# Kernel optimization log

Hardware: AMD Instinct MI355X
Metric: run time of the kernel (lower is better)

Reference implementation:

```python
import jax, jax.numpy as jnp
import numpy as np

TEMPERATURE = 0.07
EPS = 1e-12  # F.normalize clamp


def _project(x, We, be, W1, b1, W2, b2):
    # encoder Linear then projection head Linear->ReLU->Linear
    h = x @ We + be                      # [B, 512]
    h = jax.nn.relu(h @ W1 + b1)         # [B, 256]
    return h @ W2 + b2                   # [B, 128]


def _ntxent(z1, z2, t):
    B = z1.shape[0]
    z1 = z1 / jnp.maximum(jnp.linalg.norm(z1, axis=1, keepdims=True), EPS)
    z2 = z2 / jnp.maximum(jnp.linalg.norm(z2, axis=1, keepdims=True), EPS)
    reps = jnp.concatenate([z1, z2], axis=0)          # [2B, 128]
    sim = reps @ reps.T                               # [2B, 2B]
    N = 2 * B
    idx = jnp.arange(N)
    # positives: eye rolled by B along columns -> column (i+B) mod N
    pos = sim[idx, (idx + B) % N][:, None]            # [N, 1]
    # negatives: all off-diagonal entries per row, in column order
    cols = jnp.arange(N - 1)[None, :]                 # [1, N-1]
    neg_idx = cols + (cols >= idx[:, None])           # skip the diagonal
    neg = jnp.take_along_axis(sim, neg_idx, axis=1)   # [N, N-1]
    logits = jnp.concatenate([pos, neg], axis=1) / t  # [N, N]
    # cross-entropy with label 0
    return jnp.mean(jax.nn.logsumexp(logits, axis=1) - logits[:, 0])


def setup_inputs() -> dict:
    key = jax.random.key(0)
    ks = jax.random.split(key, 10)
    B, Din, Denc, Dh, Dp = 4096, 1024, 512, 256, 128
    s = lambda fan_in: 1.0 / np.sqrt(fan_in)
    return {
        "x_image": jax.random.normal(ks[0], (B, Din), jnp.float32),
        "x_text": jax.random.normal(ks[1], (B, Din), jnp.float32),
        "We_img": jax.random.normal(ks[2], (Din, Denc), jnp.float32) * s(Din),
        "be_img": jnp.zeros((Denc,), jnp.float32),
        "We_txt": jax.random.normal(ks[3], (Din, Denc), jnp.float32) * s(Din),
        "be_txt": jnp.zeros((Denc,), jnp.float32),
        "Wp1_img": jax.random.normal(ks[4], (Denc, Dh), jnp.float32) * s(Denc),
        "bp1_img": jnp.zeros((Dh,), jnp.float32),
        "Wp2_img": jax.random.normal(ks[5], (Dh, Dp), jnp.float32) * s(Dh),
        "bp2_img": jnp.zeros((Dp,), jnp.float32),
        "Wp1_txt": jax.random.normal(ks[6], (Denc, Dh), jnp.float32) * s(Denc),
        "bp1_txt": jnp.zeros((Dh,), jnp.float32),
        "Wp2_txt": jax.random.normal(ks[7], (Dh, Dp), jnp.float32) * s(Dh),
        "bp2_txt": jnp.zeros((Dp,), jnp.float32),
    }


def reference(x_image, x_text, We_img, be_img, We_txt, be_txt,
              Wp1_img, bp1_img, Wp2_img, bp2_img,
              Wp1_txt, bp1_txt, Wp2_txt, bp2_txt):
    z1 = _project(x_image, We_img, be_img, Wp1_img, bp1_img, Wp2_img, bp2_img)
    z2 = _project(x_text, We_txt, be_txt, Wp1_txt, bp1_txt, Wp2_txt, bp2_txt)
    # single modality pair ('image','text') -> one NT-Xent loss
    return _ntxent(z1, z2, TEMPERATURE)
```

## Files before the change

### kernel.cpp

```cpp
#include <hip/hip_runtime.h>
#include <hip/hip_bf16.h>
#include <math.h>

typedef __bf16 bf16_t;
typedef __bf16 bf8 __attribute__((ext_vector_type(8)));
typedef __bf16 bf4 __attribute__((ext_vector_type(4)));
typedef __bf16 bf16x2 __attribute__((ext_vector_type(2)));
typedef float f32x4 __attribute__((ext_vector_type(4)));

#define AS1 __attribute__((address_space(1)))
#define AS3 __attribute__((address_space(3)))

#define B_ROWS 4096
#define NTOT   8192
#define DIN    1024
#define DENC   512
#define DH     256
#define DP     128
#define INV_T        14.285714285714286f
#define SCALE_LOG2   20.609929155556620f

__device__ __forceinline__ f32x4 mfma_16x16x32(bf8 a, bf8 b, f32x4 c) {
  return __builtin_amdgcn_mfma_f32_16x16x32_bf16(a, b, c, 0, 0, 0);
}

__global__ __launch_bounds__(256) void prep_kernel(
    const float* __restrict__ x_i, const float* __restrict__ x_t,
    const float* __restrict__ We_i, const float* __restrict__ We_t,
    const float* __restrict__ W1_i, const float* __restrict__ W1_t,
    const float* __restrict__ W2_i, const float* __restrict__ W2_t,
    bf16_t* __restrict__ xb_i, bf16_t* __restrict__ xb_t,
    bf16_t* __restrict__ Wet_i, bf16_t* __restrict__ Wet_t,
    bf16_t* __restrict__ W1t_i, bf16_t* __restrict__ W1t_t,
    bf16_t* __restrict__ W2t_i, bf16_t* __restrict__ W2t_t) {
  const int b = blockIdx.x;
  const int tid = threadIdx.x;
  if (b >= 336) {
    int idx = (b - 336) * 256 + tid;
    const int HALF = (B_ROWS * DIN) / 4;
    const float* s; bf16_t* d; int off;
    if (idx < HALF) { s = x_i; d = xb_i; off = idx; }
    else            { s = x_t; d = xb_t; off = idx - HALF; }
    float4 v = ((const float4*)s)[off];
    bf4 w = { (bf16_t)v.x, (bf16_t)v.y, (bf16_t)v.z, (bf16_t)v.w };
    ((bf4*)d)[off] = w;
    return;
  }
  const float* src; bf16_t* dst; int K, N, tile;
  if (b < 128)      { src = We_i; dst = Wet_i; K = 1024; N = 512; tile = b; }
  else if (b < 256) { src = We_t; dst = Wet_t; K = 1024; N = 512; tile = b - 128; }
  else if (b < 288) { src = W1_i; dst = W1t_i; K = 512;  N = 256; tile = b - 256; }
  else if (b < 320) { src = W1_t; dst = W1t_t; K = 512;  N = 256; tile = b - 288; }
  else if (b < 328) { src = W2_i; dst = W2t_i; K = 256;  N = 128; tile = b - 320; }
  else              { src = W2_t; dst = W2t_t; K = 256;  N = 128; tile = b - 328; }
  const int tilesN = N >> 6;
  const int k0 = (tile / tilesN) * 64;
  const int n0 = (tile % tilesN) * 64;

  __shared__ float ld[64][65];
  #pragma unroll
  for (int i = 0; i < 4; ++i) {
    int cid = tid + i * 256;
    int r = cid >> 4;
    int c = (cid & 15) * 4;
    float4 v = *(const float4*)(src + (size_t)(k0 + r) * N + n0 + c);
    ld[r][c + 0] = v.x; ld[r][c + 1] = v.y; ld[r][c + 2] = v.z; ld[r][c + 3] = v.w;
  }
  __syncthreads();
  #pragma unroll
  for (int i = 0; i < 2; ++i) {
    int cid = tid + i * 256;
    int rn = cid >> 3;
    int c8 = (cid & 7) * 8;
    bf8 w;
    #pragma unroll
    for (int j = 0; j < 8; ++j) w[j] = (bf16_t)ld[c8 + j][rn];
    *(bf8*)(dst + (size_t)(n0 + rn) * K + k0 + c8) = w;
  }
}

template<int MT, bool RELU>
__global__ __launch_bounds__(256) void gemm_glds(
    const bf16_t* __restrict__ A0, const bf16_t* __restrict__ A1,
    const bf16_t* __restrict__ B0, const bf16_t* __restrict__ B1,
    const float* __restrict__ bias0, const float* __restrict__ bias1,
    bf16_t* __restrict__ out0, bf16_t* __restrict__ out1,
    int N, int K) {
  const bf16_t* A   = blockIdx.z ? A1 : A0;
  const bf16_t* Bt  = blockIdx.z ? B1 : B0;
  const float* bias = blockIdx.z ? bias1 : bias0;
  bf16_t* outp      = blockIdx.z ? out1 : out0;

  const int nb   = blockIdx.x * 64;
  const int mb   = blockIdx.y * MT;
  const int tid  = threadIdx.x;
  const int wave = tid >> 6;
  const int lane = tid & 63;
  const int l15  = lane & 15;
  const int quad = lane >> 4;
  constexpr int CH = MT / 64;

  __shared__ __align__(16) bf16_t As[MT * 32];
  __shared__ __align__(16) bf16_t Bs[64 * 32];

  f32x4 acc[CH][4];
  #pragma unroll
  for (int i = 0; i < CH; ++i)
    #pragma unroll
    for (int j = 0; j < 4; ++j) acc[i][j] = (f32x4){0.f, 0.f, 0.f, 0.f};

  for (int k0 = 0; k0 < K; k0 += 32) {
    __syncthreads();
    #pragma unroll
    for (int i = 0; i < CH; ++i) {
      const int s = tid + i * 256;
      const bf16_t* ga = A + (size_t)(mb + (s >> 2)) * K + k0 + (s & 3) * 8;
      __builtin_amdgcn_global_load_lds(
          (const AS1 void*)ga,
          (AS3 void*)(As + (size_t)(wave * 64 + i * 256) * 8), 16, 0, 0);
    }
    {
      const int s = tid;
      const bf16_t* gb = Bt + (size_t)(nb + (s >> 2)) * K + k0 + (s & 3) * 8;
      __builtin_amdgcn_global_load_lds(
          (const AS1 void*)gb,
          (AS3 void*)(Bs + (size_t)(wave * 64) * 8), 16, 0, 0);
    }
    __syncthreads();

    bf8 a[CH];
    #pragma unroll
    for (int i = 0; i < CH; ++i)
      a[i] = *(const bf8*)(As + (size_t)(wave * (16 * CH) + i * 16 + l15) * 32 + quad * 8);
    #pragma unroll
    for (int nt = 0; nt < 4; ++nt) {
      bf8 bb = *(const bf8*)(Bs + (size_t)(nt * 16 + l15) * 32 + quad * 8);
      #pragma unroll
      for (int i = 0; i < CH; ++i)
        acc[i][nt] = mfma_16x16x32(a[i], bb, acc[i][nt]);
    }
  }

  #pragma unroll
  for (int i = 0; i < CH; ++i) {
    const int orow = mb + wave * (16 * CH) + i * 16 + quad * 4;
    #pragma unroll
    for (int nt = 0; nt < 4; ++nt) {
      const int ocol = nb + nt * 16 + l15;
      const float bval = bias[ocol];
      #pragma unroll
      for (int r = 0; r < 4; ++r) {
        float v = acc[i][nt][r] + bval;
        if (RELU) v = fmaxf(v, 0.f);
        outp[(size_t)(orow + r) * N + ocol] = (bf16_t)v;
      }
    }
  }
}

__global__ __launch_bounds__(256) void head2_norm(
    const bf16_t* __restrict__ A0, const bf16_t* __restrict__ A1,
    const bf16_t* __restrict__ B0, const bf16_t* __restrict__ B1,
    const float* __restrict__ bias0, const float* __restrict__ bias1,
    bf16_t* __restrict__ reps) {
  const bf16_t* A   = blockIdx.z ? A1 : A0;
  const bf16_t* Bt  = blockIdx.z ? B1 : B0;
  const float* bias = blockIdx.z ? bias1 : bias0;

  const int mb   = blockIdx.x * 64;
  const int tid  = threadIdx.x;
  const int wave = tid >> 6;
  const int lane = tid & 63;
  const int l15  = lane & 15;
  const int quad = lane >> 4;

  __shared__ __align__(16) bf16_t As[64][40];
  __shared__ __align__(16) bf16_t Bs[128][40];

  f32x4 acc[8];
  #pragma unroll
  for (int i = 0; i < 8; ++i) acc[i] = (f32x4){0.f, 0.f, 0.f, 0.f};

  const int arow   = tid >> 2;
  const int achunk = (tid & 3) << 3;
  const bf16_t* Ap = A + (size_t)(mb + arow) * DH + achunk;

  for (int k0 = 0; k0 < DH; k0 += 32) {
    uint4 av = *(const uint4*)(Ap + k0);
    uint4 bv[2];
    #pragma unroll
    for (int i = 0; i < 2; ++i) {
      int cid = tid + i * 256;
      int br = cid >> 2, bc = (cid & 3) << 3;
      bv[i] = *(const uint4*)(Bt + (size_t)br * DH + k0 + bc);
    }
    __syncthreads();
    *(uint4*)&As[arow][achunk] = av;
    #pragma unroll
    for (int i = 0; i < 2; ++i) {
      int cid = tid + i * 256;
      int br = cid >> 2, bc = (cid & 3) << 3;
      *(uint4*)&Bs[br][bc] = bv[i];
    }
    __syncthreads();
    bf8 af = *(const bf8*)&As[wave * 16 + l15][quad * 8];
    #pragma unroll
    for (int nt = 0; nt < 8; ++nt) {
      bf8 bfv = *(const bf8*)&Bs[nt * 16 + l15][quad * 8];
      acc[nt] = mfma_16x16x32(af, bfv, acc[nt]);
    }
  }

  #pragma unroll
  for (int nt = 0; nt < 8; ++nt) {
    const float bval = bias[nt * 16 + l15];
    #pragma unroll
    for (int r = 0; r < 4; ++r) acc[nt][r] += bval;
  }
  const size_t rowbase = (size_t)(blockIdx.z ? B_ROWS : 0) + mb + wave * 16 + quad * 4;
  #pragma unroll
  for (int r = 0; r < 4; ++r) {
    float ss = 0.f;
    #pragma unroll
    for (int nt = 0; nt < 8; ++nt) ss += acc[nt][r] * acc[nt][r];
    ss += __shfl_xor(ss, 1);
    ss += __shfl_xor(ss, 2);
    ss += __shfl_xor(ss, 4);
    ss += __shfl_xor(ss, 8);
    const float inv = 1.0f / fmaxf(sqrtf(ss), 1e-12f);
    #pragma unroll
    for (int nt = 0; nt < 8; ++nt)
      reps[(rowbase + r) * DP + nt * 16 + l15] = (bf16_t)(acc[nt][r] * inv);
  }
}

__global__ __launch_bounds__(256) void sim_rowsum_kernel(
    const bf16_t* __restrict__ reps, float* __restrict__ S) {
  const int rowbase = blockIdx.y * 128;
  const int col0    = blockIdx.x * 512;
  const int tid  = threadIdx.x;
  const int wave = tid >> 6;
  const int lane = tid & 63;
  const int l15  = lane & 15;
  const int quad = lane >> 4;

  __shared__ __align__(16) bf16_t Bs[2][64 * DP];

  const int r0 = rowbase + wave * 32;
  bf8 af0[4], af1[4];
  #pragma unroll
  for (int kt = 0; kt < 4; ++kt) {
    af0[kt] = *(const bf8*)(reps + (size_t)(r0 + l15)      * DP + kt * 32 + quad * 8);
    af1[kt] = *(const bf8*)(reps + (size_t)(r0 + 16 + l15) * DP + kt * 32 + quad * 8);
  }

  float rs0[4] = {0.f, 0.f, 0.f, 0.f};
  float rs1[4] = {0.f, 0.f, 0.f, 0.f};

  for (int t = 0; t < 8; ++t) {
    bf16_t* buf = Bs[t & 1];
    __syncthreads();
    const int jt0 = col0 + t * 64;
    #pragma unroll
    for (int r = 0; r < 4; ++r) {
      const int s   = r * 256 + tid;
      const int col = s >> 4;
      const int cf  = (s & 15) ^ (col & 15);
      const bf16_t* g = reps + (size_t)(jt0 + col) * DP + cf * 8;
      __builtin_amdgcn_global_load_lds(
          (const AS1 void*)g,
          (AS3 void*)(buf + (size_t)(r * 256 + wave * 64) * 8), 16, 0, 0);
    }
    __syncthreads();

    #pragma unroll
    for (int st = 0; st < 4; ++st) {
      const bf16_t* base = buf + (size_t)(st * 16 + l15) * DP;
      bf8 b0 = *(const bf8*)(base + (((0 * 4 + quad) ^ l15) * 8));
      bf8 b1 = *(const bf8*)(base + (((1 * 4 + quad) ^ l15) * 8));
      bf8 b2 = *(const bf8*)(base + (((2 * 4 + quad) ^ l15) * 8));
      bf8 b3 = *(const bf8*)(base + (((3 * 4 + quad) ^ l15) * 8));
      f32x4 acc0 = (f32x4){0.f, 0.f, 0.f, 0.f};
      f32x4 acc1 = (f32x4){0.f, 0.f, 0.f, 0.f};
      acc0 = mfma_16x16x32(af0[0], b0, acc0); acc1 = mfma_16x16x32(af1[0], b0, acc1);
      acc0 = mfma_16x16x32(af0[1], b1, acc0); acc1 = mfma_16x16x32(af1[1], b1, acc1);
      acc0 = mfma_16x16x32(af0[2], b2, acc0); acc1 = mfma_16x16x32(af1[2], b2, acc1);
      acc0 = mfma_16x16x32(af0[3], b3, acc0); acc1 = mfma_16x16x32(af1[3], b3, acc1);
      #pragma unroll
      for (int r = 0; r < 4; ++r) {
        rs0[r] += __builtin_amdgcn_exp2f(acc0[r] * SCALE_LOG2);
        rs1[r] += __builtin_amdgcn_exp2f(acc1[r] * SCALE_LOG2);
      }
    }
  }

  const int i0 = r0 + quad * 4;
  #pragma unroll
  for (int r = 0; r < 4; ++r) {
    float v = rs0[r];
    v += __shfl_xor(v, 1); v += __shfl_xor(v, 2);
    v += __shfl_xor(v, 4); v += __shfl_xor(v, 8);
    if (l15 == 0) atomicAdd(&S[i0 + r], v);
  }
  #pragma unroll
  for (int r = 0; r < 4; ++r) {
    float v = rs1[r];
    v += __shfl_xor(v, 1); v += __shfl_xor(v, 2);
    v += __shfl_xor(v, 4); v += __shfl_xor(v, 8);
    if (l15 == 0) atomicAdd(&S[i0 + 16 + r], v);
  }
}

__global__ __launch_bounds__(256) void rowfinal_kernel(
    const bf16_t* __restrict__ reps, const float* __restrict__ S,
    float* __restrict__ Lsum, int* __restrict__ cnt,
    float* __restrict__ out) {
  const int tid  = threadIdx.x;
  const int wave = tid >> 6;
  const int lane = tid & 63;
  float part = 0.f;
  #pragma unroll 1
  for (int i = 0; i < 16; ++i) {
    const int row = blockIdx.x * 64 + wave * 16 + i;
    bf16x2 a = *(const bf16x2*)(reps + (size_t)row * DP + lane * 2);
    bf16x2 b = *(const bf16x2*)(reps + (size_t)(row ^ B_ROWS) * DP + lane * 2);
    float a0 = (float)a.x, a1 = (float)a.y;
    float b0 = (float)b.x, b1 = (float)b.y;
    float dii = a0 * a0 + a1 * a1;
    float pos = a0 * b0 + a1 * b1;
    #pragma unroll
    for (int m = 1; m < 64; m <<= 1) {
      dii += __shfl_xor(dii, m);
      pos += __shfl_xor(pos, m);
    }
    if (lane == 0) {
      float Si = S[row] - __builtin_amdgcn_exp2f(dii * SCALE_LOG2)
                        + __builtin_amdgcn_exp2f(pos * SCALE_LOG2);
      part += logf(Si) - pos * INV_T;
    }
  }
  __shared__ float wpart[4];
  if (lane == 0) wpart[wave] = part;
  __syncthreads();
  if (tid == 0) {
    float bsum = wpart[0] + wpart[1] + wpart[2] + wpart[3];
    atomicAdd(Lsum, bsum);
    __threadfence();
    int old = __hip_atomic_fetch_add(cnt, 1, __ATOMIC_ACQ_REL,
                                     __HIP_MEMORY_SCOPE_AGENT);
    if (old == (int)gridDim.x - 1) {
      float tot = __hip_atomic_load(Lsum, __ATOMIC_RELAXED,
                                    __HIP_MEMORY_SCOPE_AGENT);
      out[0] = tot * (1.0f / NTOT);
    }
  }
}

extern "C" void kernel_launch(void* const* d_in, const int* in_sizes, int n_in,
                              void* d_out, int out_size, void* d_ws, size_t ws_size,
                              hipStream_t stream) {
  const float* x_img  = (const float*)d_in[0];
  const float* x_txt  = (const float*)d_in[1];
  const float* We_img = (const float*)d_in[2];
  const float* be_img = (const float*)d_in[3];
  const float* We_txt = (const float*)d_in[4];
  const float* be_txt = (const float*)d_in[5];
  const float* W1_img = (const float*)d_in[6];
  const float* b1_img = (const float*)d_in[7];
  const float* W2_img = (const float*)d_in[8];
  const float* b2_img = (const float*)d_in[9];
  const float* W1_txt = (const float*)d_in[10];
  const float* b1_txt = (const float*)d_in[11];
  const float* W2_txt = (const float*)d_in[12];
  const float* b2_txt = (const float*)d_in[13];

  char* p = (char*)d_ws;
  bf16_t* xbf_img = (bf16_t*)p; p += (size_t)B_ROWS * DIN * 2;
  bf16_t* xbf_txt = (bf16_t*)p; p += (size_t)B_ROWS * DIN * 2;
  bf16_t* Wet_img = (bf16_t*)p; p += (size_t)DENC * DIN * 2;
  bf16_t* Wet_txt = (bf16_t*)p; p += (size_t)DENC * DIN * 2;
  bf16_t* W1t_img = (bf16_t*)p; p += (size_t)DH * DENC * 2;
  bf16_t* W1t_txt = (bf16_t*)p; p += (size_t)DH * DENC * 2;
  bf16_t* W2t_img = (bf16_t*)p; p += (size_t)DP * DH * 2;
  bf16_t* W2t_txt = (bf16_t*)p; p += (size_t)DP * DH * 2;
  bf16_t* h_img   = (bf16_t*)p; p += (size_t)B_ROWS * DENC * 2;
  bf16_t* h_txt   = (bf16_t*)p; p += (size_t)B_ROWS * DENC * 2;
  bf16_t* g_img   = (bf16_t*)p; p += (size_t)B_ROWS * DH * 2;
  bf16_t* g_txt   = (bf16_t*)p; p += (size_t)B_ROWS * DH * 2;
  bf16_t* reps    = (bf16_t*)p; p += (size_t)NTOT * DP * 2;
  float*  S       = (float*) p; p += (size_t)NTOT * 4;
  float*  Lsum    = (float*) p; p += 4;
  int*    cnt     = (int*)   p; p += 4;

  hipMemsetAsync(S, 0, (size_t)NTOT * 4 + 8, stream);

  prep_kernel<<<336 + 8192, 256, 0, stream>>>(
      x_img, x_txt, We_img, We_txt, W1_img, W1_txt, W2_img, W2_txt,
      xbf_img, xbf_txt, Wet_img, Wet_txt, W1t_img, W1t_txt, W2t_img, W2t_txt);

  gemm_glds<128, false><<<dim3(DENC / 64, B_ROWS / 128, 2), 256, 0, stream>>>(
      xbf_img, xbf_txt, Wet_img, Wet_txt, be_img, be_txt, h_img, h_txt,
      DENC, DIN);
  gemm_glds<64, true><<<dim3(DH / 64, B_ROWS / 64, 2), 256, 0, stream>>>(
      h_img, h_txt, W1t_img, W1t_txt, b1_img, b1_txt, g_img, g_txt,
      DH, DENC);
  head2_norm<<<dim3(B_ROWS / 64, 1, 2), 256, 0, stream>>>(
      g_img, g_txt, W2t_img, W2t_txt, b2_img, b2_txt, reps);

  sim_rowsum_kernel<<<dim3(16, NTOT / 128), 256, 0, stream>>>(reps, S);
  rowfinal_kernel<<<NTOT / 64, 256, 0, stream>>>(reps, S, Lsum, cnt,
                                                 (float*)d_out);
}
```

Baseline: 191.8 us.

## Double-buffer GEMM and sim tiles, fuse row-final reduction into sim kernel

The projection GEMM and the similarity row-sum kernel now prefetch the next K or column tile into a second LDS buffer while the current tile is being multiplied. This is meant to hide global-to-LDS load latency behind MFMA work. The separate row-final kernel and the memset are removed. The sim kernel instead writes per-slice partial row sums, and the last-arriving block for each row block, found through an atomic counter, computes that block's loss terms. Counters and the loss accumulator are zeroed in the prep kernel, which relies on the workspace layout placing Lsum directly after the counters.

```diff
diff --git a/kernel.cpp b/kernel.cpp
--- a/kernel.cpp
+++ b/kernel.cpp
@@ -17,6 +17,7 @@
 #define DENC   512
 #define DH     256
 #define DP     128
+#define NSLICE 16
 #define INV_T        14.285714285714286f
 #define SCALE_LOG2   20.609929155556620f
 
@@ -32,7 +33,8 @@
     bf16_t* __restrict__ xb_i, bf16_t* __restrict__ xb_t,
     bf16_t* __restrict__ Wet_i, bf16_t* __restrict__ Wet_t,
     bf16_t* __restrict__ W1t_i, bf16_t* __restrict__ W1t_t,
-    bf16_t* __restrict__ W2t_i, bf16_t* __restrict__ W2t_t) {
+    bf16_t* __restrict__ W2t_i, bf16_t* __restrict__ W2t_t,
+    int* __restrict__ Ctr) {
   const int b = blockIdx.x;
   const int tid = threadIdx.x;
   if (b >= 336) {
@@ -46,6 +48,7 @@
     ((bf4*)d)[off] = w;
     return;
   }
+  if (b == 0 && tid < 66) Ctr[tid] = 0;
   const float* src; bf16_t* dst; int K, N, tile;
   if (b < 128)      { src = We_i; dst = Wet_i; K = 1024; N = 512; tile = b; }
   else if (b < 256) { src = We_t; dst = Wet_t; K = 1024; N = 512; tile = b - 128; }
@@ -100,8 +103,8 @@
   const int quad = lane >> 4;
   constexpr int CH = MT / 64;
 
-  __shared__ __align__(16) bf16_t As[MT * 32];
-  __shared__ __align__(16) bf16_t Bs[64 * 32];
+  __shared__ __align__(16) bf16_t As[2][MT * 32];
+  __shared__ __align__(16) bf16_t Bs[2][64 * 32];
 
   f32x4 acc[CH][4];
   #pragma unroll
@@ -109,32 +112,35 @@
     #pragma unroll
     for (int j = 0; j < 4; ++j) acc[i][j] = (f32x4){0.f, 0.f, 0.f, 0.f};
 
-  for (int k0 = 0; k0 < K; k0 += 32) {
-    __syncthreads();
+  auto stage = [&](int k0, int pb) {
     #pragma unroll
     for (int i = 0; i < CH; ++i) {
       const int s = tid + i * 256;
       const bf16_t* ga = A + (size_t)(mb + (s >> 2)) * K + k0 + (s & 3) * 8;
       __builtin_amdgcn_global_load_lds(
           (const AS1 void*)ga,
-          (AS3 void*)(As + (size_t)(wave * 64 + i * 256) * 8), 16, 0, 0);
-    }
-    {
-      const int s = tid;
-      const bf16_t* gb = Bt + (size_t)(nb + (s >> 2)) * K + k0 + (s & 3) * 8;
-      __builtin_amdgcn_global_load_lds(
-          (const AS1 void*)gb,
-          (AS3 void*)(Bs + (size_t)(wave * 64) * 8), 16, 0, 0);
-    }
+          (AS3 void*)(As[pb] + (size_t)(wave * 64 + i * 256) * 8), 16, 0, 0);
+    }
+    const bf16_t* gb = Bt + (size_t)(nb + (tid >> 2)) * K + k0 + (tid & 3) * 8;
+    __builtin_amdgcn_global_load_lds(
+        (const AS1 void*)gb,
+        (AS3 void*)(Bs[pb] + (size_t)(wave * 64) * 8), 16, 0, 0);
+  };
+
+  stage(0, 0);
+  const int T = K >> 5;
+  for (int t = 0; t < T; ++t) {
     __syncthreads();
-
+    if (t + 1 < T) stage((t + 1) << 5, (t + 1) & 1);
+    const bf16_t* as = As[t & 1];
+    const bf16_t* bs = Bs[t & 1];
     bf8 a[CH];
     #pragma unroll
     for (int i = 0; i < CH; ++i)
-      a[i] = *(const bf8*)(As + (size_t)(wave * (16 * CH) + i * 16 + l15) * 32 + quad * 8);
+      a[i] = *(const bf8*)(as + (size_t)(wave * (16 * CH) + i * 16 + l15) * 32 + quad * 8);
     #pragma unroll
     for (int nt = 0; nt < 4; ++nt) {
-      bf8 bb = *(const bf8*)(Bs + (size_t)(nt * 16 + l15) * 32 + quad * 8);
+      bf8 bb = *(const bf8*)(bs + (size_t)(nt * 16 + l15) * 32 + quad * 8);
       #pragma unroll
       for (int i = 0; i < CH; ++i)
         acc[i][nt] = mfma_16x16x32(a[i], bb, acc[i][nt]);
@@ -235,9 +241,13 @@
 }
 
 __global__ __launch_bounds__(256) void sim_rowsum_kernel(
-    const bf16_t* __restrict__ reps, float* __restrict__ S) {
-  const int rowbase = blockIdx.y * 128;
-  const int col0    = blockIdx.x * 512;
+    const bf16_t* __restrict__ reps, float* __restrict__ Spart,
+    int* __restrict__ Ctr, float* __restrict__ Lsum,
+    float* __restrict__ out) {
+  const int rowblock = blockIdx.y;
+  const int rowbase  = rowblock * 128;
+  const int slice    = blockIdx.x;
+  const int col0     = slice * 512;
   const int tid  = threadIdx.x;
   const int wave = tid >> 6;
   const int lane = tid & 63;
@@ -245,6 +255,8 @@
   const int quad = lane >> 4;
 
   __shared__ __align__(16) bf16_t Bs[2][64 * DP];
+  __shared__ int lastFlag;
+  __shared__ float wpart[4];
 
   const int r0 = rowbase + wave * 32;
   bf8 af0[4], af1[4];
@@ -257,9 +269,7 @@
   float rs0[4] = {0.f, 0.f, 0.f, 0.f};
   float rs1[4] = {0.f, 0.f, 0.f, 0.f};
 
-  for (int t = 0; t < 8; ++t) {
-    bf16_t* buf = Bs[t & 1];
-    __syncthreads();
+  auto stage = [&](int t, int pb) {
     const int jt0 = col0 + t * 64;
     #pragma unroll
     for (int r = 0; r < 4; ++r) {
@@ -269,10 +279,15 @@
       const bf16_t* g = reps + (size_t)(jt0 + col) * DP + cf * 8;
       __builtin_amdgcn_global_load_lds(
           (const AS1 void*)g,
-          (AS3 void*)(buf + (size_t)(r * 256 + wave * 64) * 8), 16, 0, 0);
-    }
+          (AS3 void*)(Bs[pb] + (size_t)(r * 256 + wave * 64) * 8), 16, 0, 0);
+    }
+  };
+
+  stage(0, 0);
+  for (int t = 0; t < 8; ++t) {
     __syncthreads();
-
+    if (t < 7) stage(t + 1, (t + 1) & 1);
+    const bf16_t* buf = Bs[t & 1];
     #pragma unroll
     for (int st = 0; st < 4; ++st) {
       const bf16_t* base = buf + (size_t)(st * 16 + l15) * DP;
@@ -300,55 +315,59 @@
     float v = rs0[r];
     v += __shfl_xor(v, 1); v += __shfl_xor(v, 2);
     v += __shfl_xor(v, 4); v += __shfl_xor(v, 8);
-    if (l15 == 0) atomicAdd(&S[i0 + r], v);
+    if (l15 == 0) Spart[(size_t)slice * NTOT + i0 + r] = v;
   }
   #pragma unroll
   for (int r = 0; r < 4; ++r) {
     float v = rs1[r];
     v += __shfl_xor(v, 1); v += __shfl_xor(v, 2);
     v += __shfl_xor(v, 4); v += __shfl_xor(v, 8);
-    if (l15 == 0) atomicAdd(&S[i0 + 16 + r], v);
-  }
-}
-
-__global__ __launch_bounds__(256) void rowfinal_kernel(
-    const bf16_t* __restrict__ reps, const float* __restrict__ S,
-    float* __restrict__ Lsum, int* __restrict__ cnt,
-    float* __restrict__ out) {
-  const int tid  = threadIdx.x;
-  const int wave = tid >> 6;
-  const int lane = tid & 63;
+    if (l15 == 0) Spart[(size_t)slice * NTOT + i0 + 16 + r] = v;
+  }
+
+  __threadfence();
+  __syncthreads();
+  if (tid == 0) {
+    int old = __hip_atomic_fetch_add(&Ctr[rowblock], 1, __ATOMIC_ACQ_REL,
+                                     __HIP_MEMORY_SCOPE_AGENT);
+    lastFlag = (old == NSLICE - 1);
+  }
+  __syncthreads();
+  if (!lastFlag) return;
+
+  __threadfence();
   float part = 0.f;
   #pragma unroll 1
-  for (int i = 0; i < 16; ++i) {
-    const int row = blockIdx.x * 64 + wave * 16 + i;
+  for (int i = 0; i < 32; ++i) {
+    const int row = rowbase + wave * 32 + i;
     bf16x2 a = *(const bf16x2*)(reps + (size_t)row * DP + lane * 2);
     bf16x2 b = *(const bf16x2*)(reps + (size_t)(row ^ B_ROWS) * DP + lane * 2);
     float a0 = (float)a.x, a1 = (float)a.y;
     float b0 = (float)b.x, b1 = (float)b.y;
     float dii = a0 * a0 + a1 * a1;
     float pos = a0 * b0 + a1 * b1;
+    float ps  = (lane < NSLICE) ? Spart[(size_t)lane * NTOT + row] : 0.f;
     #pragma unroll
     for (int m = 1; m < 64; m <<= 1) {
       dii += __shfl_xor(dii, m);
       pos += __shfl_xor(pos, m);
+      ps  += __shfl_xor(ps, m);
     }
     if (lane == 0) {
-      float Si = S[row] - __builtin_amdgcn_exp2f(dii * SCALE_LOG2)
-                        + __builtin_amdgcn_exp2f(pos * SCALE_LOG2);
+      float Si = ps - __builtin_amdgcn_exp2f(dii * SCALE_LOG2)
+                    + __builtin_amdgcn_exp2f(pos * SCALE_LOG2);
       part += logf(Si) - pos * INV_T;
     }
   }
-  __shared__ float wpart[4];
   if (lane == 0) wpart[wave] = part;
   __syncthreads();
   if (tid == 0) {
     float bsum = wpart[0] + wpart[1] + wpart[2] + wpart[3];
     atomicAdd(Lsum, bsum);
     __threadfence();
-    int old = __hip_atomic_fetch_add(cnt, 1, __ATOMIC_ACQ_REL,
+    int old = __hip_atomic_fetch_add(&Ctr[64], 1, __ATOMIC_ACQ_REL,
                                      __HIP_MEMORY_SCOPE_AGENT);
-    if (old == (int)gridDim.x - 1) {
+    if (old == 63) {
       float tot = __hip_atomic_load(Lsum, __ATOMIC_RELAXED,
                                     __HIP_MEMORY_SCOPE_AGENT);
       out[0] = tot * (1.0f / NTOT);
@@ -388,15 +407,14 @@
   bf16_t* g_img   = (bf16_t*)p; p += (size_t)B_ROWS * DH * 2;
   bf16_t* g_txt   = (bf16_t*)p; p += (size_t)B_ROWS * DH * 2;
   bf16_t* reps    = (bf16_t*)p; p += (size_t)NTOT * DP * 2;
-  float*  S       = (float*) p; p += (size_t)NTOT * 4;
+  float*  Spart   = (float*) p; p += (size_t)NSLICE * NTOT * 4;
+  int*    Ctr     = (int*)   p; p += 65 * 4;
   float*  Lsum    = (float*) p; p += 4;
-  int*    cnt     = (int*)   p; p += 4;
-
-  hipMemsetAsync(S, 0, (size_t)NTOT * 4 + 8, stream);
 
   prep_kernel<<<336 + 8192, 256, 0, stream>>>(
       x_img, x_txt, We_img, We_txt, W1_img, W1_txt, W2_img, W2_txt,
-      xbf_img, xbf_txt, Wet_img, Wet_txt, W1t_img, W1t_txt, W2t_img, W2t_txt);
+      xbf_img, xbf_txt, Wet_img, Wet_txt, W1t_img, W1t_txt, W2t_img, W2t_txt,
+      Ctr);
 
   gemm_glds<128, false><<<dim3(DENC / 64, B_ROWS / 128, 2), 256, 0, stream>>>(
       xbf_img, xbf_txt, Wet_img, Wet_txt, be_img, be_txt, h_img, h_txt,
@@ -407,7 +425,6 @@
   head2_norm<<<dim3(B_ROWS / 64, 1, 2), 256, 0, stream>>>(
       g_img, g_txt, W2t_img, W2t_txt, b2_img, b2_txt, reps);
 
-  sim_rowsum_kernel<<<dim3(16, NTOT / 128), 256, 0, stream>>>(reps, S);
-  rowfinal_kernel<<<NTOT / 64, 256, 0, stream>>>(reps, S, Lsum, cnt,
-                                                 (float*)d_out);
-}
+  sim_rowsum_kernel<<<dim3(NSLICE, NTOT / 128), 256, 0, stream>>>(
+      reps, Spart, Ctr, Lsum, (float*)d_out);
+}
```

Result: slower. 334.2 us (+74.2%).
